# Optimization experiments

Measured on AMD Instinct MI355X. Metric: run time of the kernel, lower is better.

Reference implementation:

```python
import jax, jax.numpy as jnp
import numpy as np

C = 512
QK = C // 8  # 64
B, L = 8, 4096


def setup_inputs() -> dict:
    key = jax.random.key(0)
    ks = jax.random.split(key, 8)
    s = 0.02
    return {
        "x": jax.random.normal(ks[0], (B, C, L), dtype=jnp.float32),
        "Wq": jax.random.normal(ks[1], (QK, C), dtype=jnp.float32) * s,
        "bq": jax.random.normal(ks[2], (QK,), dtype=jnp.float32) * s,
        "Wk": jax.random.normal(ks[3], (QK, C), dtype=jnp.float32) * s,
        "bk": jax.random.normal(ks[4], (QK,), dtype=jnp.float32) * s,
        "Wv": jax.random.normal(ks[5], (C, C), dtype=jnp.float32) * s,
        "bv": jax.random.normal(ks[6], (C,), dtype=jnp.float32) * s,
        "gamma": jax.random.normal(ks[7], (1,), dtype=jnp.float32) * 0.1,
    }


def reference(x, Wq, bq, Wk, bk, Wv, bv, gamma):
    # 1x1 convs are per-position linear projections over channels
    q = jnp.einsum('bcl,dc->bld', x, Wq) + bq            # [B, L, QK]  (proj_query, permuted)
    k = jnp.einsum('bcl,dc->bdl', x, Wk) + bk[:, None]   # [B, QK, L]  (proj_key)
    v = jnp.einsum('bcl,dc->bdl', x, Wv) + bv[:, None]   # [B, C, L]   (proj_value)
    energy = jnp.einsum('bid,bdj->bij', q, k)            # [B, L, L]
    attn = jax.nn.softmax(energy, axis=-1)               # softmax over j
    out = jnp.einsum('bcj,bij->bci', v, attn)            # [B, C, L]
    return gamma * out + x
```

## Files before the change

### kernel.cpp

```cpp
#include <hip/hip_runtime.h>
#include <math.h>

#define BB 8
#define CC 512
#define LL 4096
#define DQK 64

typedef short short8 __attribute__((ext_vector_type(8)));
typedef unsigned short ushort4v __attribute__((ext_vector_type(4)));
typedef unsigned short ushort8v __attribute__((ext_vector_type(8)));
typedef float floatx4 __attribute__((ext_vector_type(4)));
typedef unsigned int uint4v __attribute__((ext_vector_type(4)));

__device__ __forceinline__ unsigned short f2bf(float f) {
    union { float f; unsigned u; } v; v.f = f;
    unsigned r = v.u + 0x7fffu + ((v.u >> 16) & 1u);
    return (unsigned short)(r >> 16);
}

__device__ __forceinline__ void load_lds16(const void* gptr, void* lptr) {
    __builtin_amdgcn_global_load_lds(
        (const __attribute__((address_space(1))) unsigned int*)gptr,
        (__attribute__((address_space(3))) unsigned int*)lptr, 16, 0, 0);
}

__device__ __forceinline__ unsigned cvt_pk_bf16(float lo, float hi) {
    unsigned r;
    asm("v_cvt_pk_bf16_f32 %0, %1, %2" : "=v"(r) : "v"(lo), "v"(hi));
    return r;
}

__global__ __launch_bounds__(256) void k_transpose(const float* __restrict__ x,
                                                   unsigned short* __restrict__ xt) {
    __shared__ unsigned short tile[64][72];
    int l0 = blockIdx.x * 64, c0 = blockIdx.y * 64, b = blockIdx.z;
    int t = threadIdx.x;
    int r  = t >> 2;
    int ch = (t & 3) * 16;
    const float* src = x + ((size_t)b * CC + c0 + r) * LL + l0 + ch;
#pragma unroll
    for (int j = 0; j < 4; ++j) {
        floatx4 v = *(const floatx4*)(src + j * 4);
        ushort4v u = { f2bf(v[0]), f2bf(v[1]), f2bf(v[2]), f2bf(v[3]) };
        *(ushort4v*)(&tile[r][ch + j * 4]) = u;
    }
    __syncthreads();
    int lr  = t >> 2;
    int cch = (t & 3) * 16;
    ushort8v o0, o1;
#pragma unroll
    for (int j = 0; j < 8; ++j) o0[j] = tile[cch + j][lr];
#pragma unroll
    for (int j = 0; j < 8; ++j) o1[j] = tile[cch + 8 + j][lr];
    unsigned short* dst = xt + ((size_t)b * LL + l0 + lr) * CC + c0 + cch;
    *(ushort8v*)(dst)     = o0;
    *(ushort8v*)(dst + 8) = o1;
}

__global__ void k_castw(const float* __restrict__ wq, const float* __restrict__ wk,
                        const float* __restrict__ wv,
                        unsigned short* __restrict__ wqb, unsigned short* __restrict__ wkb,
                        unsigned short* __restrict__ wvb) {
    int i = blockIdx.x * 256 + threadIdx.x;
    if (i < DQK * CC) { wqb[i] = f2bf(wq[i]); wkb[i] = f2bf(wk[i]); }
    wvb[i] = f2bf(wv[i]);
}

__global__ __launch_bounds__(256) void k_projall(const unsigned short* __restrict__ xt,
                                                 const unsigned short* __restrict__ wqb,
                                                 const unsigned short* __restrict__ wkb,
                                                 const unsigned short* __restrict__ wvb,
                                                 const float* __restrict__ bq,
                                                 const float* __restrict__ bk,
                                                 const float* __restrict__ bv,
                                                 unsigned short* __restrict__ qout,
                                                 unsigned short* __restrict__ kout,
                                                 unsigned short* __restrict__ vout) {
    int l0 = blockIdx.x * 64;
    int b  = blockIdx.y;
    int tid = threadIdx.x;
    int w = tid >> 6, lane = tid & 63;
    int lane16 = lane & 15, g = lane >> 4;
    __shared__ unsigned short xtile[64 * 512];
    {
        const unsigned short* xg = xt + ((size_t)b * LL + l0) * CC;
        int pg = tid & 63;
#pragma unroll
        for (int ci = 0; ci < 16; ++ci) {
            int r  = ci * 4 + (tid >> 6);
            int sg = (pg & 56) | ((pg ^ r) & 7);
            load_lds16(xg + (size_t)r * CC + sg * 8, xtile + ((size_t)ci * 256 + tid) * 8);
        }
    }

    int xe = (g ^ (lane16 & 7)) * 8;
    int xo = ((g + 4) ^ (lane16 & 7)) * 8;

    auto loadW8 = [&](short8 (&af)[8], int hs) {
        int z = hs >> 1, kh = hs & 1;
        const unsigned short* base;
        if (z < 8)       base = wvb + (size_t)(z * 64 + w * 16 + lane16) * CC;
        else if (z == 8) base = wqb + (size_t)(w * 16 + lane16) * CC;
        else             base = wkb + (size_t)(w * 16 + lane16) * CC;
        base += g * 8 + kh * 256;
#pragma unroll
        for (int kk = 0; kk < 8; ++kk) af[kk] = *(const short8*)(base + kk * 32);
    };

    short8 wA[8], wB[8];
    loadW8(wA, 0);
    __syncthreads();

    for (int z = 0; z < 10; ++z) {
        loadW8(wB, z * 2 + 1);
        floatx4 acc[4];
#pragma unroll
        for (int nt = 0; nt < 4; ++nt) acc[nt] = {0.f, 0.f, 0.f, 0.f};
#pragma unroll
        for (int nt = 0; nt < 4; ++nt)
#pragma unroll
            for (int kk = 0; kk < 8; ++kk) {
                int off = (nt * 16 + lane16) * 512 + (kk >> 1) * 64 + ((kk & 1) ? xo : xe);
                short8 bfrag = *(const short8*)(xtile + off);
                acc[nt] = __builtin_amdgcn_mfma_f32_16x16x32_bf16(wA[kk], bfrag, acc[nt], 0, 0, 0);
            }
        if (z + 1 < 10) loadW8(wA, (z + 1) * 2);
#pragma unroll
        for (int nt = 0; nt < 4; ++nt)
#pragma unroll
            for (int kk = 0; kk < 8; ++kk) {
                int kk8 = kk + 8;
                int off = (nt * 16 + lane16) * 512 + (kk8 >> 1) * 64 + ((kk8 & 1) ? xo : xe);
                short8 bfrag = *(const short8*)(xtile + off);
                acc[nt] = __builtin_amdgcn_mfma_f32_16x16x32_bf16(wB[kk], bfrag, acc[nt], 0, 0, 0);
            }
#pragma unroll
        for (int nt = 0; nt < 4; ++nt) {
            int l = l0 + nt * 16 + lane16;
            if (z < 8) {
#pragma unroll
                for (int r = 0; r < 4; ++r) {
                    int d = z * 64 + w * 16 + g * 4 + r;
                    vout[((size_t)b * CC + d) * LL + l] = f2bf(acc[nt][r] + bv[d]);
                }
            } else {
                const float* bias = (z == 8) ? bq : bk;
                float sc = (z == 8) ? 1.4426950408889634f : 1.0f;
                ushort4v o;
#pragma unroll
                for (int r = 0; r < 4; ++r)
                    o[r] = f2bf((acc[nt][r] + bias[w * 16 + g * 4 + r]) * sc);
                unsigned short* dst = ((z == 8) ? qout : kout)
                                      + ((size_t)b * LL + l) * DQK + w * 16 + g * 4;
                *(ushort4v*)dst = o;
            }
        }
    }
}

__global__ __launch_bounds__(256, 2) void k_attn(const unsigned short* __restrict__ q,
                                                 const unsigned short* __restrict__ kws,
                                                 const unsigned short* __restrict__ vws,
                                                 const float* __restrict__ x,
                                                 const float* __restrict__ gamma,
                                                 float* __restrict__ out) {
    int bid = blockIdx.x + 32 * blockIdx.y + 256 * blockIdx.z;
    int x8  = bid & 7;
    int ii  = bid >> 3;
    int wg  = (x8 + 8 * (ii >> 5)) * 32 + (ii & 31);
    int i0 = (wg & 31) * 128;
    int b  = (wg >> 5) & 7;
    int c0 = (wg >> 8) * 256;

    int tid = threadIdx.x;
    int w = tid >> 6, lane = tid & 63;
    int lane16 = lane & 15, g = lane >> 4;
    int iw = i0 + w * 32;

    __shared__ unsigned short kt[2][64 * 64];
    __shared__ unsigned short vt[2][256 * 64];

    short8 qf[2][2];
#pragma unroll
    for (int m = 0; m < 2; ++m) {
        const unsigned short* qrow = q + ((size_t)b * LL + iw + m * 16 + lane16) * DQK + g * 8;
        qf[m][0] = *(const short8*)(qrow);
        qf[m][1] = *(const short8*)(qrow + 32);
    }

    const unsigned short* kglob = kws + (size_t)b * LL * DQK;
    const unsigned short* vglob = vws + ((size_t)b * CC + c0) * LL;
    int gr    = (tid & 7) ^ ((tid >> 3) & 7);
    int koff0 = (tid >> 3) * DQK + gr * 8;
    int voff0 = (tid >> 3) * LL  + gr * 8;

    int kro[2], vro[2];
#pragma unroll
    for (int kk = 0; kk < 2; ++kk) {
        int sw = (kk * 4 + g) ^ (lane16 & 7);
        kro[kk] = lane16 * 64 + sw * 8;
        vro[kk] = lane16 * 64 + sw * 8;
    }

    short8 ones;
#pragma unroll
    for (int j = 0; j < 8; ++j) ones[j] = (short)0x3f80;

    floatx4 O[2][16];
#pragma unroll
    for (int m = 0; m < 2; ++m)
#pragma unroll
        for (int nt = 0; nt < 16; ++nt) O[m][nt] = {0.f, 0.f, 0.f, 0.f};
    floatx4 Ol[2];
#pragma unroll
    for (int m = 0; m < 2; ++m) Ol[m] = {0.f, 0.f, 0.f, 0.f};

    auto stageK = [&](int j0n, int buf) {
        const unsigned short* ks = kglob + j0n * DQK + koff0;
        unsigned short* kd = &kt[buf][tid * 8];
        load_lds16(ks,        kd);
        load_lds16(ks + 2048, kd + 2048);
    };
    auto stageV = [&](int j0n, int buf) {
        const unsigned short* vs = vglob + j0n + voff0;
        unsigned short* vd = &vt[buf][tid * 8];
#pragma unroll
        for (int i = 0; i < 8; ++i)
            load_lds16(vs + i * 131072, vd + i * 2048);
    };

    auto softmax_half = [&](floatx4 (&Sh)[2][2], short8 (&paD)[2]) {
#pragma unroll
        for (int m = 0; m < 2; ++m) {
            float e0[4], e1[4];
#pragma unroll
            for (int r = 0; r < 4; ++r) {
                e0[r] = __builtin_amdgcn_exp2f(Sh[m][0][r]);
                e1[r] = __builtin_amdgcn_exp2f(Sh[m][1][r]);
            }
            unsigned A0 = cvt_pk_bf16(e0[0], e0[1]);
            unsigned A1 = cvt_pk_bf16(e0[2], e0[3]);
            unsigned B0 = cvt_pk_bf16(e1[0], e1[1]);
            unsigned B1 = cvt_pk_bf16(e1[2], e1[3]);
            asm("v_permlane32_swap_b32 %0, %1" : "+v"(A0), "+v"(B0));
            asm("v_permlane16_swap_b32 %0, %1" : "+v"(A0), "+v"(B0));
            asm("v_permlane32_swap_b32 %0, %1" : "+v"(A1), "+v"(B1));
            asm("v_permlane16_swap_b32 %0, %1" : "+v"(A1), "+v"(B1));
            uint4v pw = { A0, A1, B0, B1 };
            paD[m] = *(short8*)&pw;
            Ol[m] = __builtin_amdgcn_mfma_f32_16x16x32_bf16(paD[m], ones, Ol[m], 0, 0, 0);
        }
    };

    stageK(0, 0);
    stageV(0, 0);
    int cur = 0;
    for (int j0 = 0; j0 < LL; j0 += 64) {
        bool more = (j0 + 64 < LL);

        asm volatile("s_waitcnt vmcnt(8)" ::: "memory");
        __builtin_amdgcn_s_barrier();
        if (more) { stageK(j0 + 64, cur ^ 1); stageV(j0 + 64, cur ^ 1); }

        const unsigned short* kbp = kt[cur];
        const unsigned short* vbp = vt[cur];

        floatx4 Sa[2][2], Sb[2][2];
#pragma unroll
        for (int m = 0; m < 2; ++m)
#pragma unroll
            for (int nt = 0; nt < 2; ++nt) { Sa[m][nt] = {0.f,0.f,0.f,0.f}; Sb[m][nt] = {0.f,0.f,0.f,0.f}; }

        short8 ka0 = *(const short8*)(kbp + kro[0]);
        short8 ka1 = *(const short8*)(kbp + kro[1]);
        short8 kb0 = *(const short8*)(kbp + kro[0] + 1024);
        short8 kb1 = *(const short8*)(kbp + kro[1] + 1024);
#pragma unroll
        for (int m = 0; m < 2; ++m) {
            Sa[m][0] = __builtin_amdgcn_mfma_f32_16x16x32_bf16(ka0, qf[m][0], Sa[m][0], 0, 0, 0);
            Sa[m][0] = __builtin_amdgcn_mfma_f32_16x16x32_bf16(ka1, qf[m][1], Sa[m][0], 0, 0, 0);
            Sa[m][1] = __builtin_amdgcn_mfma_f32_16x16x32_bf16(kb0, qf[m][0], Sa[m][1], 0, 0, 0);
            Sa[m][1] = __builtin_amdgcn_mfma_f32_16x16x32_bf16(kb1, qf[m][1], Sa[m][1], 0, 0, 0);
        }
        short8 kc0 = *(const short8*)(kbp + kro[0] + 2048);
        short8 kc1 = *(const short8*)(kbp + kro[1] + 2048);
        short8 kd0 = *(const short8*)(kbp + kro[0] + 3072);
        short8 kd1 = *(const short8*)(kbp + kro[1] + 3072);
#pragma unroll
        for (int m = 0; m < 2; ++m) {
            Sb[m][0] = __builtin_amdgcn_mfma_f32_16x16x32_bf16(kc0, qf[m][0], Sb[m][0], 0, 0, 0);
            Sb[m][0] = __builtin_amdgcn_mfma_f32_16x16x32_bf16(kc1, qf[m][1], Sb[m][0], 0, 0, 0);
            Sb[m][1] = __builtin_amdgcn_mfma_f32_16x16x32_bf16(kd0, qf[m][0], Sb[m][1], 0, 0, 0);
            Sb[m][1] = __builtin_amdgcn_mfma_f32_16x16x32_bf16(kd1, qf[m][1], Sb[m][1], 0, 0, 0);
        }

        short8 pa0[2], pa1[2];
        softmax_half(Sa, pa0);

        if (more) asm volatile("s_waitcnt vmcnt(10)" ::: "memory");
        else      asm volatile("s_waitcnt vmcnt(0)"  ::: "memory");
        __builtin_amdgcn_s_barrier();

        __builtin_amdgcn_s_setprio(1);
#pragma unroll
        for (int nt = 0; nt < 8; ++nt) {
            short8 vf = *(const short8*)(vbp + vro[0] + nt * 1024);
#pragma unroll
            for (int m = 0; m < 2; ++m)
                O[m][nt] = __builtin_amdgcn_mfma_f32_16x16x32_bf16(pa0[m], vf, O[m][nt], 0, 0, 0);
        }
        __builtin_amdgcn_s_setprio(0);

        softmax_half(Sb, pa1);

        __builtin_amdgcn_s_setprio(1);
#pragma unroll
        for (int nt = 8; nt < 16; ++nt) {
            short8 vf = *(const short8*)(vbp + vro[0] + nt * 1024);
#pragma unroll
            for (int m = 0; m < 2; ++m)
                O[m][nt] = __builtin_amdgcn_mfma_f32_16x16x32_bf16(pa0[m], vf, O[m][nt], 0, 0, 0);
        }
#pragma unroll
        for (int nt = 0; nt < 16; ++nt) {
            short8 vf = *(const short8*)(vbp + vro[1] + nt * 1024);
#pragma unroll
            for (int m = 0; m < 2; ++m)
                O[m][nt] = __builtin_amdgcn_mfma_f32_16x16x32_bf16(pa1[m], vf, O[m][nt], 0, 0, 0);
        }
        __builtin_amdgcn_s_setprio(0);
        cur ^= 1;
    }

    float linv[2][4];
#pragma unroll
    for (int m = 0; m < 2; ++m)
#pragma unroll
        for (int r = 0; r < 4; ++r) linv[m][r] = 1.f / Ol[m][r];

    float gam = gamma[0];
#pragma unroll
    for (int m = 0; m < 2; ++m)
#pragma unroll
        for (int nt = 0; nt < 16; ++nt) {
            int c = c0 + nt * 16 + lane16;
            size_t base = ((size_t)b * CC + c) * LL + iw + m * 16 + g * 4;
            floatx4 xv = *(const floatx4*)(x + base);
            floatx4 o;
#pragma unroll
            for (int r = 0; r < 4; ++r) o[r] = gam * (O[m][nt][r] * linv[m][r]) + xv[r];
            *(floatx4*)(out + base) = o;
        }
}

extern "C" void kernel_launch(void* const* d_in, const int* in_sizes, int n_in,
                              void* d_out, int out_size, void* d_ws, size_t ws_size,
                              hipStream_t stream) {
    const float* x     = (const float*)d_in[0];
    const float* Wq    = (const float*)d_in[1];
    const float* bq    = (const float*)d_in[2];
    const float* Wk    = (const float*)d_in[3];
    const float* bk    = (const float*)d_in[4];
    const float* Wv    = (const float*)d_in[5];
    const float* bv    = (const float*)d_in[6];
    const float* gamma = (const float*)d_in[7];
    float* out = (float*)d_out;

    unsigned short* xt  = (unsigned short*)d_ws;
    unsigned short* qb  = xt  + (size_t)BB * LL * CC;
    unsigned short* kb  = qb  + (size_t)BB * LL * DQK;
    unsigned short* vb  = kb  + (size_t)BB * LL * DQK;
    unsigned short* wqb = vb  + (size_t)BB * CC * LL;
    unsigned short* wkb = wqb + (size_t)DQK * CC;
    unsigned short* wvb = wkb + (size_t)DQK * CC;

    k_transpose<<<dim3(LL / 64, CC / 64, BB), 256, 0, stream>>>(x, xt);
    k_castw<<<dim3((CC * CC) / 256), 256, 0, stream>>>(Wq, Wk, Wv, wqb, wkb, wvb);
    k_projall<<<dim3(LL / 64, BB), 256, 0, stream>>>(xt, wqb, wkb, wvb, bq, bk, bv, qb, kb, vb);
    k_attn<<<dim3(LL / 128, BB, CC / 256), 256, 0, stream>>>(qb, kb, vb, x, gamma, out);
}
```

Baseline: 359.3 us.

## Fuse x transpose/cast into projection kernel and simplify attention staging sync

Removes the separate transpose kernel. The projection kernel now reads fp32 x directly, converts it to bf16 and scatters it into the swizzled LDS tile, which saves one global round-trip of the transposed activations and one launch. The attention loop also replaces its fine-grained vmcnt waits and two barriers per iteration with a single __syncthreads before prefetching the next K/V tile. The LDS writes are scalar 2-byte scatters that may bank-conflict, and the coarser sync may reduce load/compute overlap.

```diff
diff --git a/kernel.cpp b/kernel.cpp
--- a/kernel.cpp
+++ b/kernel.cpp
@@ -28,33 +28,6 @@
     unsigned r;
     asm("v_cvt_pk_bf16_f32 %0, %1, %2" : "=v"(r) : "v"(lo), "v"(hi));
     return r;
-}
-
-__global__ __launch_bounds__(256) void k_transpose(const float* __restrict__ x,
-                                                   unsigned short* __restrict__ xt) {
-    __shared__ unsigned short tile[64][72];
-    int l0 = blockIdx.x * 64, c0 = blockIdx.y * 64, b = blockIdx.z;
-    int t = threadIdx.x;
-    int r  = t >> 2;
-    int ch = (t & 3) * 16;
-    const float* src = x + ((size_t)b * CC + c0 + r) * LL + l0 + ch;
-#pragma unroll
-    for (int j = 0; j < 4; ++j) {
-        floatx4 v = *(const floatx4*)(src + j * 4);
-        ushort4v u = { f2bf(v[0]), f2bf(v[1]), f2bf(v[2]), f2bf(v[3]) };
-        *(ushort4v*)(&tile[r][ch + j * 4]) = u;
-    }
-    __syncthreads();
-    int lr  = t >> 2;
-    int cch = (t & 3) * 16;
-    ushort8v o0, o1;
-#pragma unroll
-    for (int j = 0; j < 8; ++j) o0[j] = tile[cch + j][lr];
-#pragma unroll
-    for (int j = 0; j < 8; ++j) o1[j] = tile[cch + 8 + j][lr];
-    unsigned short* dst = xt + ((size_t)b * LL + l0 + lr) * CC + c0 + cch;
-    *(ushort8v*)(dst)     = o0;
-    *(ushort8v*)(dst + 8) = o1;
 }
 
 __global__ void k_castw(const float* __restrict__ wq, const float* __restrict__ wk,
@@ -66,30 +39,42 @@
     wvb[i] = f2bf(wv[i]);
 }
 
-__global__ __launch_bounds__(256) void k_projall(const unsigned short* __restrict__ xt,
-                                                 const unsigned short* __restrict__ wqb,
-                                                 const unsigned short* __restrict__ wkb,
-                                                 const unsigned short* __restrict__ wvb,
-                                                 const float* __restrict__ bq,
-                                                 const float* __restrict__ bk,
-                                                 const float* __restrict__ bv,
-                                                 unsigned short* __restrict__ qout,
-                                                 unsigned short* __restrict__ kout,
-                                                 unsigned short* __restrict__ vout) {
+__global__ __launch_bounds__(256) void k_prep(const float* __restrict__ x,
+                                              const unsigned short* __restrict__ wqb,
+                                              const unsigned short* __restrict__ wkb,
+                                              const unsigned short* __restrict__ wvb,
+                                              const float* __restrict__ bq,
+                                              const float* __restrict__ bk,
+                                              const float* __restrict__ bv,
+                                              unsigned short* __restrict__ qout,
+                                              unsigned short* __restrict__ kout,
+                                              unsigned short* __restrict__ vout) {
     int l0 = blockIdx.x * 64;
     int b  = blockIdx.y;
     int tid = threadIdx.x;
     int w = tid >> 6, lane = tid & 63;
     int lane16 = lane & 15, g = lane >> 4;
     __shared__ unsigned short xtile[64 * 512];
+
     {
-        const unsigned short* xg = xt + ((size_t)b * LL + l0) * CC;
-        int pg = tid & 63;
-#pragma unroll
-        for (int ci = 0; ci < 16; ++ci) {
-            int r  = ci * 4 + (tid >> 6);
-            int sg = (pg & 56) | ((pg ^ r) & 7);
-            load_lds16(xg + (size_t)r * CC + sg * 8, xtile + ((size_t)ci * 256 + tid) * 8);
+        int cr = tid >> 2;
+        int ch = (tid & 3) * 16;
+#pragma unroll
+        for (int cc = 0; cc < 8; ++cc) {
+            int c  = cc * 64 + cr;
+            int gc = c >> 3;
+            int cl = c & 7;
+            const float* src = x + ((size_t)b * CC + c) * LL + l0 + ch;
+#pragma unroll
+            for (int j = 0; j < 4; ++j) {
+                floatx4 v = *(const floatx4*)(src + j * 4);
+#pragma unroll
+                for (int e = 0; e < 4; ++e) {
+                    int l  = ch + j * 4 + e;
+                    int pg = (gc & 56) | ((gc ^ (l & 7)) & 7);
+                    xtile[l * 512 + pg * 8 + cl] = f2bf(v[e]);
+                }
+            }
         }
     }
 
@@ -215,13 +200,11 @@
 #pragma unroll
     for (int m = 0; m < 2; ++m) Ol[m] = {0.f, 0.f, 0.f, 0.f};
 
-    auto stageK = [&](int j0n, int buf) {
+    auto stage = [&](int j0n, int buf) {
         const unsigned short* ks = kglob + j0n * DQK + koff0;
         unsigned short* kd = &kt[buf][tid * 8];
         load_lds16(ks,        kd);
         load_lds16(ks + 2048, kd + 2048);
-    };
-    auto stageV = [&](int j0n, int buf) {
         const unsigned short* vs = vglob + j0n + voff0;
         unsigned short* vd = &vt[buf][tid * 8];
 #pragma unroll
@@ -252,15 +235,11 @@
         }
     };
 
-    stageK(0, 0);
-    stageV(0, 0);
+    stage(0, 0);
     int cur = 0;
     for (int j0 = 0; j0 < LL; j0 += 64) {
-        bool more = (j0 + 64 < LL);
-
-        asm volatile("s_waitcnt vmcnt(8)" ::: "memory");
-        __builtin_amdgcn_s_barrier();
-        if (more) { stageK(j0 + 64, cur ^ 1); stageV(j0 + 64, cur ^ 1); }
+        __syncthreads();
+        if (j0 + 64 < LL) stage(j0 + 64, cur ^ 1);
 
         const unsigned short* kbp = kt[cur];
         const unsigned short* vbp = vt[cur];
@@ -296,10 +275,6 @@
 
         short8 pa0[2], pa1[2];
         softmax_half(Sa, pa0);
-
-        if (more) asm volatile("s_waitcnt vmcnt(10)" ::: "memory");
-        else      asm volatile("s_waitcnt vmcnt(0)"  ::: "memory");
-        __builtin_amdgcn_s_barrier();
 
         __builtin_amdgcn_s_setprio(1);
 #pragma unroll
@@ -366,16 +341,14 @@
     const float* gamma = (const float*)d_in[7];
     float* out = (float*)d_out;
 
-    unsigned short* xt  = (unsigned short*)d_ws;
-    unsigned short* qb  = xt  + (size_t)BB * LL * CC;
+    unsigned short* qb  = (unsigned short*)d_ws;
     unsigned short* kb  = qb  + (size_t)BB * LL * DQK;
     unsigned short* vb  = kb  + (size_t)BB * LL * DQK;
     unsigned short* wqb = vb  + (size_t)BB * CC * LL;
     unsigned short* wkb = wqb + (size_t)DQK * CC;
     unsigned short* wvb = wkb + (size_t)DQK * CC;
 
-    k_transpose<<<dim3(LL / 64, CC / 64, BB), 256, 0, stream>>>(x, xt);
     k_castw<<<dim3((CC * CC) / 256), 256, 0, stream>>>(Wq, Wk, Wv, wqb, wkb, wvb);
-    k_projall<<<dim3(LL / 64, BB), 256, 0, stream>>>(xt, wqb, wkb, wvb, bq, bk, bv, qb, kb, vb);
+    k_prep<<<dim3(LL / 64, BB), 256, 0, stream>>>(x, wqb, wkb, wvb, bq, bk, bv, qb, kb, vb);
     k_attn<<<dim3(LL / 128, BB, CC / 256), 256, 0, stream>>>(qb, kb, vb, x, gamma, out);
 }
```

Result: faster. 339.7 us (-5.5%).
